# Performance work log

Measured on AMD Instinct MI355X. Metric: run time of the kernel, lower is better.

## Reference

```python
import jax, jax.numpy as jnp
import numpy as np

K = 3          # kernel_size per pseudo-coordinate dim
DIM = 3        # edge_attr dimensionality
M = K ** DIM   # total number of spline kernel weight matrices


def spline_conv(x, src, dst, pseudo, W, Wr, b):
    """Degree-1 open B-spline conv (torch_geometric SplineConv, aggr='mean').
    x: (N, C_in), pseudo: (E, DIM) in [0,1], W: (M, C_in, C_out), Wr: (C_in, C_out), b: (C_out,).
    """
    N, C_in = x.shape
    pos = pseudo * (K - 1)                      # (E, DIM) in [0, K-1]
    i0 = jnp.clip(jnp.floor(pos), 0, K - 2)     # lower knot index per dim
    frac = pos - i0                             # (E, DIM) linear basis fraction
    i0 = i0.astype(jnp.int32)
    strides = jnp.array([1, K, K * K], dtype=jnp.int32)
    xj = x[src]                                 # (E, C_in) irregular gather
    # accumulate basis-weighted neighbor features per (dst node, kernel index)
    acc = jnp.zeros((N * M, C_in), dtype=x.dtype)
    for bits in range(2 ** DIM):                # 8 corners of the linear B-spline support
        off = jnp.array([(bits >> d) & 1 for d in range(DIM)], dtype=jnp.int32)
        w = jnp.prod(jnp.where(off == 1, frac, 1.0 - frac), axis=1)       # (E,)
        kidx = jnp.sum((i0 + off[None, :]) * strides[None, :], axis=1)    # (E,) flat kernel idx
        acc = acc.at[dst * M + kidx].add(w[:, None] * xj)                 # scatter-add
    out = jnp.einsum('nmi,mio->no', acc.reshape(N, M, C_in), W)
    deg = jnp.zeros((N,), x.dtype).at[dst].add(1.0)                        # in-degree
    out = out / jnp.maximum(deg, 1.0)[:, None]                             # mean aggregation
    return out + x @ Wr + b                                                # root weight + bias


def setup_inputs() -> dict:
    key = jax.random.key(0)
    ks = jax.random.split(key, 16)
    N, E = 50000, 800000
    dims = [3, 64, 64, 64]
    inp = {
        "x": jax.random.normal(ks[0], (N, 3), jnp.float32),
        "edge_index": jax.random.randint(ks[1], (2, E), 0, N),
        "edge_attr": jax.random.uniform(ks[2], (E, DIM), dtype=jnp.float32),
    }
    for l in range(3):
        ci, co = dims[l], dims[l + 1]
        inp[f"W{l}"] = jax.random.normal(ks[3 + 3 * l], (M, ci, co), jnp.float32) * (1.0 / np.sqrt(ci * M))
        inp[f"root{l}"] = jax.random.normal(ks[4 + 3 * l], (ci, co), jnp.float32) * (1.0 / np.sqrt(ci))
        inp[f"b{l}"] = jnp.zeros((co,), jnp.float32)
    return inp


def reference(x, edge_index, edge_attr, W0, root0, b0, W1, root1, b1, W2, root2, b2):
    src, dst = edge_index[0], edge_index[1]   # PyG flow: source_to_target
    h = x
    for W, Wr, b in ((W0, root0, b0), (W1, root1, b1), (W2, root2, b2)):
        h = jax.nn.relu(spline_conv(h, src, dst, edge_attr, W, Wr, b))
    return h
```

## Files before the change

### kernel.cpp

```cpp
#include <hip/hip_runtime.h>
#include <cstdint>


typedef __attribute__((ext_vector_type(8))) short short8;
typedef __attribute__((ext_vector_type(4))) float floatx4;

#define AS1 __attribute__((address_space(1)))
#define AS3 __attribute__((address_space(3)))

__device__ inline short f2bf(float f) {
    union { float f; unsigned u; } x; x.f = f;
    unsigned r = x.u + 0x7FFF + ((x.u >> 16) & 1);
    return (short)(r >> 16);
}

__device__ inline float bf2f(unsigned short u) {
    union { unsigned u; float f; } x;
    x.u = ((unsigned)u) << 16;
    return x.f;
}


__global__ void count_kernel(const int* __restrict__ ei, int* __restrict__ count, int E) {
    int e = blockIdx.x * blockDim.x + threadIdx.x;
    if (e < E) atomicAdd(&count[ei[E + e]], 1);
}

__global__ __launch_bounds__(1024) void scan_tile_kernel(const int* __restrict__ count,
                                                         int* __restrict__ row_ptr,
                                                         int* __restrict__ bsum, int N) {
    __shared__ int wsum[16];
    int tid = threadIdx.x, lane = tid & 63, wid = tid >> 6;
    int i = blockIdx.x * 1024 + tid;
    int v = (i < N) ? count[i] : 0;
    int incl = v;
#pragma unroll
    for (int off = 1; off < 64; off <<= 1) {
        int t = __shfl_up(incl, off, 64);
        if (lane >= off) incl += t;
    }
    if (lane == 63) wsum[wid] = incl;
    __syncthreads();
    if (tid < 16) {
        int w = wsum[tid];
#pragma unroll
        for (int off = 1; off < 16; off <<= 1) {
            int t = __shfl_up(w, off, 16);
            if ((tid & 15) >= off) w += t;
        }
        wsum[tid] = w;
    }
    __syncthreads();
    int waveoff = (wid > 0) ? wsum[wid - 1] : 0;
    if (i < N) row_ptr[i] = waveoff + incl - v;
    if (tid == 1023) bsum[blockIdx.x] = waveoff + incl;
}

__global__ __launch_bounds__(64) void scan_bsum_kernel(const int* __restrict__ bsum,
                                                       int* __restrict__ boff,
                                                       int* __restrict__ tot, int nb) {
    int tid = threadIdx.x;
    int v = (tid < nb) ? bsum[tid] : 0;
    int incl = v;
#pragma unroll
    for (int off = 1; off < 64; off <<= 1) {
        int t = __shfl_up(incl, off, 64);
        if (tid >= off) incl += t;
    }
    boff[tid] = incl - v;
    if (tid == 63) tot[0] = incl;
}

__global__ __launch_bounds__(1024) void scan_add_kernel(int* __restrict__ row_ptr,
                                                        const int* __restrict__ boff,
                                                        const int* __restrict__ tot,
                                                        int* __restrict__ cursor, int N) {
    int i = blockIdx.x * 1024 + threadIdx.x;
    if (i < N) {
        int r = row_ptr[i] + boff[blockIdx.x];
        row_ptr[i] = r;
        cursor[i] = r;
    }
    if (i == 0) row_ptr[N] = tot[0];
}

__global__ void basis_sort_kernel(const int* __restrict__ ei, const float* __restrict__ attr,
                                  const int* __restrict__ count, int* __restrict__ cursor,
                                  int* __restrict__ s_meta, float* __restrict__ s_w,
                                  unsigned short* __restrict__ s_wcol, int E) {
    int e = blockIdx.x * blockDim.x + threadIdx.x;
    if (e >= E) return;
    int src = ei[e];
    int dst = ei[E + e];
    float f[3]; int i0[3];
#pragma unroll
    for (int d = 0; d < 3; d++) {
        float pos = attr[e * 3 + d] * 2.0f;
        float fl = floorf(pos);
        fl = fminf(fmaxf(fl, 0.0f), 1.0f);
        i0[d] = (int)fl;
        f[d] = pos - fl;
    }
    int base = i0[0] + 3 * i0[1] + 9 * i0[2];
    float invd = 1.0f / fmaxf((float)count[dst], 1.0f);
    int p = atomicAdd(&cursor[dst], 1);
    s_meta[p] = src | (base << 24);
    float w[8];
#pragma unroll
    for (int c = 0; c < 8; c++) {
        float ww = invd;
#pragma unroll
        for (int d = 0; d < 3; d++) {
            int off = (c >> d) & 1;
            ww *= off ? f[d] : (1.0f - f[d]);
        }
        w[c] = ww;
    }
    floatx4 w03 = {w[0], w[1], w[2], w[3]};
    floatx4 w47 = {w[4], w[5], w[6], w[7]};
    *(floatx4*)(s_w + (size_t)p * 8) = w03;
    *(floatx4*)(s_w + (size_t)p * 8 + 4) = w47;
    unsigned short* wc = s_wcol + (size_t)p * 32;
    short8 z8 = {0, 0, 0, 0, 0, 0, 0, 0};
    *(short8*)(wc) = z8;
    *(short8*)(wc + 8) = z8;
    *(short8*)(wc + 16) = z8;
    *(short8*)(wc + 24) = z8;
#pragma unroll
    for (int c = 0; c < 8; c++) {
        int coff = (c & 1) + 3 * ((c >> 1) & 1) + 9 * (c >> 2);
        wc[base + coff] = (unsigned short)f2bf(w[c]);
    }
}

__global__ void build_wb2(const float* __restrict__ Wa, const float* __restrict__ Ra,
                          unsigned short* __restrict__ wba,
                          const float* __restrict__ Wb, const float* __restrict__ Rb,
                          unsigned short* __restrict__ wbb) {
    int idx0 = blockIdx.x * blockDim.x + threadIdx.x;
    int half = idx0 / (4 * 56 * 64);
    if (half >= 2) return;
    int idx = idx0 - half * (4 * 56 * 64);
    const float* W = half ? Wb : Wa;
    const float* Wr = half ? Rb : Ra;
    unsigned short* wb = half ? wbb : wba;
    int l = idx & 63;
    int c = (idx >> 6) % 56;
    int t = idx / (56 * 64);
    int q = l >> 4, o = t * 16 + (l & 15);
    short8 out;
#pragma unroll
    for (int j = 0; j < 8; j++) {
        int k = c * 32 + q * 8 + j;
        float v = (k < 1728) ? W[(size_t)k * 64 + o] : Wr[(size_t)(k - 1728) * 64 + o];
        out[j] = f2bf(v);
    }
    *(short8*)(wb + (size_t)idx * 8) = out;
}

__global__ __launch_bounds__(256) void layer0_kernel(
    const float* __restrict__ x, const float* __restrict__ W0,
    const float* __restrict__ Wr, const float* __restrict__ bias,
    const int* __restrict__ row_ptr, const int* __restrict__ s_meta,
    const float* __restrict__ s_w, unsigned short* __restrict__ h_out, int N) {
    constexpr int NPB = 32, KT = 84;
    __shared__ __align__(16) float acc[NPB * 2 * KT];
    int tid = threadIdx.x, lane = tid & 63, wv = tid >> 6;
    int n0 = blockIdx.x * NPB;
    for (int k = tid; k < NPB * 2 * KT; k += 256) acc[k] = 0.0f;
    __syncthreads();

    int d = lane >> 5, hl = lane & 31;
    int c = hl / 3, i = hl - c * 3;
    bool act = (hl < 24);
    int cc = act ? c : 0;
    int coff = (c & 1) + 3 * ((c >> 1) & 1) + 9 * (c >> 2);

    for (int g2 = 0; g2 < 8; g2++) {
        int g = wv * 8 + g2;
        int n = n0 + g;
        if (n >= N) continue;
        if (lane < 3) acc[(g * 2) * KT + 81 + lane] = x[(size_t)n * 3 + lane];
        int rs = row_ptr[n], re = row_ptr[n + 1];
        int npairs = (re - rs + 1) >> 1;
        float* accd = &acc[(g * 2 + d) * KT];
        for (int pb = 0; pb < npairs; pb += 4) {
            int metas[4]; float ws_[4], xs_[4];
#pragma unroll
            for (int j = 0; j < 4; j++) {
                int ej = rs + (pb + j) * 2 + d;
                bool v = (pb + j < npairs) && (ej < re);
                int ec = v ? ej : rs;
                metas[j] = s_meta[ec];
                float wv_ = s_w[(size_t)ec * 8 + cc];
                ws_[j] = v ? wv_ : 0.0f;
            }
#pragma unroll
            for (int j = 0; j < 4; j++)
                xs_[j] = x[(size_t)(metas[j] & 0xFFFFFF) * 3 + i];
#pragma unroll
            for (int j = 0; j < 4; j++) {
                int kidx = ((metas[j] >> 24) & 0xF) + coff;
                if (act) accd[kidx * 3 + i] += ws_[j] * xs_[j];
            }
        }
    }
    __syncthreads();

    int o = lane;
    float wreg[KT];
#pragma unroll
    for (int k = 0; k < KT; k++)
        wreg[k] = (k < 81) ? W0[k * 64 + o] : Wr[(k - 81) * 64 + o];
    float bv = bias[o];
    for (int g = wv; g < NPB; g += 4) {
        int n = n0 + g;
        if (n >= N) break;
        float s = bv;
#pragma unroll
        for (int k4 = 0; k4 < KT; k4 += 4) {
            floatx4 a0 = *(const floatx4*)&acc[(g * 2) * KT + k4];
            floatx4 a1 = *(const floatx4*)&acc[(g * 2 + 1) * KT + k4];
            s += (a0.x + a1.x) * wreg[k4] + (a0.y + a1.y) * wreg[k4 + 1]
               + (a0.z + a1.z) * wreg[k4 + 2] + (a0.w + a1.w) * wreg[k4 + 3];
        }
        h_out[(size_t)n * 64 + o] = (unsigned short)f2bf(fmaxf(s, 0.0f));
    }
}

template <bool OUTF32>
__global__ __launch_bounds__(512, 4) void layer64_kernel(
    const unsigned short* __restrict__ h_in, const unsigned short* __restrict__ wb,
    const float* __restrict__ bias, const int* __restrict__ row_ptr,
    const int* __restrict__ s_meta, const unsigned short* __restrict__ s_wcol,
    const unsigned short* __restrict__ zpad, void* __restrict__ h_out, int N) {
    constexpr int NPB = 8;
    constexpr int RGS = 3216;
    __shared__ __align__(16) unsigned short lds[NPB * RGS];
    int tid = threadIdx.x, lane = tid & 63;
    int wvu = __builtin_amdgcn_readfirstlane(tid >> 6);
    int n0 = blockIdx.x * NPB;
    int srow = lane & 15, sgrp = lane >> 4;

    unsigned short* reg = &lds[(size_t)wvu * RGS];
    unsigned short* featL = reg;
    unsigned short* wcolL = reg + 2048;
    int* metaL = (int*)(reg + 3072);

#define STAGE_WCOL(CB) do { \
    _Pragma("unroll") for (int k = 0; k < 2; k++) { \
        int el = (CB) + k * 16 + (lane >> 2); \
        const unsigned short* srcp = (el < dw) \
            ? s_wcol + (size_t)(rs + wbo + el) * 32 + (lane & 3) * 8 \
            : zpad + (lane & 3) * 8; \
        __builtin_amdgcn_global_load_lds((const AS1 unsigned int*)srcp, \
            (AS3 unsigned int*)(wcolL + k * 512), 16, 0, 0); \
    } \
} while (0)

    {
        int n = n0 + wvu;
        if (n >= N) {
            for (int k = lane; k < 1792; k += 64) reg[k] = 0;
        } else {
            {
                short8 z = {0, 0, 0, 0, 0, 0, 0, 0};
#pragma unroll
                for (int s = 0; s < 4; s++)
                    *(short8*)(featL + lane * 8 + s * 512) = z;
            }
            floatx4 facc[2][4];
#pragma unroll
            for (int mt = 0; mt < 2; mt++)
#pragma unroll
                for (int nt = 0; nt < 4; nt++)
                    facc[mt][nt] = (floatx4){0.0f, 0.0f, 0.0f, 0.0f};

            int rs = row_ptr[n], re = row_ptr[n + 1];
            int deg = re - rs;
            for (int wbo = 0; wbo < deg; wbo += 64) {
                int dw = deg - wbo;
                __builtin_amdgcn_global_load_lds(
                    (const AS1 unsigned int*)(s_meta + rs + wbo + lane),
                    (AS3 unsigned int*)metaL, 4, 0, 0);
                STAGE_WCOL(0);
                asm volatile("s_waitcnt vmcnt(0)" ::: "memory");
                int vmax = (dw < 64 ? dw : 64) - 1;
                for (int ch2 = 0; ch2 < 2; ch2++) {
                    int cb = ch2 * 32;
                    if (cb >= dw) break;
                    int nsl = dw - cb; if (nsl > 32) nsl = 32;
                    int ngl = (nsl + 7) >> 3;
                    for (int i = 0; i < ngl; i++) {
                        int el = cb + i * 8 + (lane >> 3);
                        if (el > vmax) el = vmax;
                        int ms = metaL[el] & 0xFFFFFF;
                        int c3 = (lane & 7) ^ (i << 1);
                        const unsigned short* srcp = h_in + (size_t)ms * 64 + c3 * 8;
                        __builtin_amdgcn_global_load_lds(
                            (const AS1 unsigned int*)srcp,
                            (AS3 unsigned int*)(featL + i * 512), 16, 0, 0);
                    }
                    short8 af0, af1;
                    {
                        const unsigned short* wrp = wcolL + (8 * sgrp) * 32 + srow;
#pragma unroll
                        for (int j = 0; j < 8; j++) {
                            af0[j] = (short)wrp[j * 32];
                            af1[j] = (short)wrp[j * 32 + 16];
                        }
                    }
                    if (ch2 == 0 && dw > 32) {
                        asm volatile("s_waitcnt lgkmcnt(0)" ::: "memory");
                        __builtin_amdgcn_sched_barrier(0);
                        STAGE_WCOL(32);
                    }
                    asm volatile("s_waitcnt vmcnt(0)" ::: "memory");
#pragma unroll
                    for (int nt = 0; nt < 4; nt++) {
                        short8 bn;
#pragma unroll
                        for (int jj = 0; jj < 8; jj++) {
                            int e = sgrp * 8 + jj;
                            int g = e * 8 + (((nt * 2) + (srow >> 3)) ^ (sgrp << 1));
                            bn[jj] = (short)featL[g * 8 + (srow & 7)];
                        }
                        facc[0][nt] = __builtin_amdgcn_mfma_f32_16x16x32_bf16(
                            af0, bn, facc[0][nt], 0, 0, 0);
                        facc[1][nt] = __builtin_amdgcn_mfma_f32_16x16x32_bf16(
                            af1, bn, facc[1][nt], 0, 0, 0);
                    }
                }
            }
#pragma unroll
            for (int mt = 0; mt < 2; mt++)
#pragma unroll
                for (int nt = 0; nt < 4; nt++)
#pragma unroll
                    for (int r = 0; r < 4; r++) {
                        int mrow = mt * 16 + sgrp * 4 + r;
                        if (mrow < 27)
                            reg[mrow * 64 + nt * 16 + srow] =
                                (unsigned short)f2bf(facc[mt][nt][r]);
                    }
            reg[1728 + lane] = h_in[(size_t)n * 64 + lane];
        }
    }
#undef STAGE_WCOL
    __syncthreads();

    {
        floatx4 f0 = {0.0f, 0.0f, 0.0f, 0.0f};
        floatx4 f1 = {0.0f, 0.0f, 0.0f, 0.0f};
        if (wvu < 4) {
            int hf = wvu >> 1;
            int tp = wvu & 1;
            const unsigned short* ap = lds + (size_t)(lane & 7) * RGS + ((lane >> 4) * 8);
            const unsigned short* wbp0 = wb + ((size_t)((tp * 2) * 56) * 64 + lane) * 8;
            const unsigned short* wbp1 = wb + ((size_t)((tp * 2 + 1) * 56) * 64 + lane) * 8;
#pragma unroll
            for (int ci = 0; ci < 28; ci++) {
                int c = hf * 28 + ci;
                short8 af = *(const short8*)(ap + c * 32);
                short8 b0 = *(const short8*)(wbp0 + (size_t)c * 64 * 8);
                short8 b1 = *(const short8*)(wbp1 + (size_t)c * 64 * 8);
                f0 = __builtin_amdgcn_mfma_f32_16x16x32_bf16(af, b0, f0, 0, 0, 0);
                f1 = __builtin_amdgcn_mfma_f32_16x16x32_bf16(af, b1, f1, 0, 0, 0);
            }
        }
        __syncthreads();
        if (wvu < 4) {
            float* pfw = (float*)(lds + (size_t)wvu * RGS);
#pragma unroll
            for (int r = 0; r < 4; r++) {
                pfw[r * 64 + lane] = f0[r];
                pfw[256 + r * 64 + lane] = f1[r];
            }
        }
        __syncthreads();
        if (wvu < 4) {
            int t = wvu;
            int o = t * 16 + (lane & 15);
            float bv = bias[o];
            const float* pfA = (const float*)(lds + (size_t)(t >> 1) * RGS)
                             + (t & 1) * 256;
            const float* pfB = (const float*)(lds + (size_t)(2 + (t >> 1)) * RGS)
                             + (t & 1) * 256;
#pragma unroll
            for (int r = 0; r < 4; r++) {
                int m = (lane >> 4) * 4 + r;
                if (m < 8) {
                    int n = n0 + m;
                    if (n < N) {
                        float s = pfA[r * 64 + lane] + pfB[r * 64 + lane];
                        float val = fmaxf(s + bv, 0.0f);
                        if (OUTF32) {
                            ((float*)h_out)[(size_t)n * 64 + o] = val;
                        } else {
                            ((unsigned short*)h_out)[(size_t)n * 64 + o] =
                                (unsigned short)f2bf(val);
                        }
                    }
                }
            }
        }
    }
}

extern "C" void kernel_launch(void* const* d_in, const int* in_sizes, int n_in,
                              void* d_out, int out_size, void* d_ws, size_t ws_size,
                              hipStream_t stream) {
    (void)n_in; (void)out_size; (void)ws_size;
    const float* x    = (const float*)d_in[0];
    const int*   ei   = (const int*)d_in[1];
    const float* attr = (const float*)d_in[2];
    const float* W0 = (const float*)d_in[3];
    const float* R0 = (const float*)d_in[4];
    const float* B0 = (const float*)d_in[5];
    const float* W1 = (const float*)d_in[6];
    const float* R1 = (const float*)d_in[7];
    const float* B1 = (const float*)d_in[8];
    const float* W2 = (const float*)d_in[9];
    const float* R2 = (const float*)d_in[10];
    const float* B2 = (const float*)d_in[11];
    const int N = in_sizes[0] / 3;
    const int E = in_sizes[1] / 2;

    char* ws = (char*)d_ws;
    size_t off = 0;
    auto alloc = [&](size_t bytes) {
        size_t cur = off;
        off = (off + bytes + 255) & ~(size_t)255;
        return cur;
    };
    int* row_ptr = (int*)(ws + alloc((size_t)(N + 1) * 4));
    int* count   = (int*)(ws + alloc((size_t)N * 4));
    int* cursor  = (int*)(ws + alloc((size_t)N * 4));
    int* bsum    = (int*)(ws + alloc(64 * 4));
    int* boff    = (int*)(ws + alloc(64 * 4));
    int* tot     = (int*)(ws + alloc(4));
    unsigned short* zpad = (unsigned short*)(ws + alloc(256));
    int* s_meta  = (int*)(ws + alloc((size_t)E * 4));
    float* s_w   = (float*)(ws + alloc((size_t)E * 8 * 4));
    unsigned short* s_wcol = (unsigned short*)(ws + alloc((size_t)E * 32 * 2));
    unsigned short* h_a  = (unsigned short*)(ws + alloc((size_t)N * 64 * 2));
    unsigned short* h_b  = (unsigned short*)(ws + alloc((size_t)N * 64 * 2));
    unsigned short* wb1  = (unsigned short*)(ws + alloc((size_t)4 * 56 * 64 * 8 * 2));
    unsigned short* wb2  = (unsigned short*)(ws + alloc((size_t)4 * 56 * 64 * 8 * 2));

    int nb = (N + 1023) / 1024;

    hipMemsetAsync(count, 0, (size_t)N * 4, stream);
    hipMemsetAsync(zpad, 0, 256, stream);
    count_kernel<<<(E + 255) / 256, 256, 0, stream>>>(ei, count, E);
    scan_tile_kernel<<<nb, 1024, 0, stream>>>(count, row_ptr, bsum, N);
    scan_bsum_kernel<<<1, 64, 0, stream>>>(bsum, boff, tot, nb);
    scan_add_kernel<<<nb, 1024, 0, stream>>>(row_ptr, boff, tot, cursor, N);
    basis_sort_kernel<<<(E + 255) / 256, 256, 0, stream>>>(ei, attr, count, cursor,
                                                           s_meta, s_w, s_wcol, E);
    build_wb2<<<(2 * 4 * 56 * 64 + 255) / 256, 256, 0, stream>>>(W1, R1, wb1,
                                                                 W2, R2, wb2);

    layer0_kernel<<<(N + 31) / 32, 256, 0, stream>>>(x, W0, R0, B0, row_ptr,
                                                     s_meta, s_w, h_a, N);
    layer64_kernel<false><<<(N + 7) / 8, 512, 0, stream>>>(h_a, wb1, B1, row_ptr,
                                                           s_meta, s_wcol, zpad, h_b, N);
    layer64_kernel<true><<<(N + 7) / 8, 512, 0, stream>>>(h_b, wb2, B2, row_ptr,
                                                          s_meta, s_wcol, zpad, d_out, N);
}
```

Measured before the change: 394.5 us.

## Fuse three-kernel scan into one block and drop fp32 edge weight buffer

Replaces the three-kernel prefix scan (tile scan, block-sum scan, add) with a single-block kernel where each thread serially sums and then writes a contiguous chunk of counts. It also stops writing the fp32 per-edge basis weights (32 bytes per edge) in the sort kernel. Layer 0 instead reads its weight from the bf16 dense s_wcol array using the kernel base index, which cuts write traffic and two launches. In exchange, layer 0 uses bf16-rounded weights, and the single-block scan does strided per-thread reads that coalesce poorly.

```diff
diff --git a/kernel.cpp b/kernel.cpp
--- a/kernel.cpp
+++ b/kernel.cpp
@@ -26,14 +26,19 @@
     if (e < E) atomicAdd(&count[ei[E + e]], 1);
 }
 
-__global__ __launch_bounds__(1024) void scan_tile_kernel(const int* __restrict__ count,
+__global__ __launch_bounds__(1024) void scan_full_kernel(const int* __restrict__ count,
                                                          int* __restrict__ row_ptr,
-                                                         int* __restrict__ bsum, int N) {
+                                                         int* __restrict__ cursor, int N) {
     __shared__ int wsum[16];
     int tid = threadIdx.x, lane = tid & 63, wid = tid >> 6;
-    int i = blockIdx.x * 1024 + tid;
-    int v = (i < N) ? count[i] : 0;
-    int incl = v;
+    int per = (N + 1023) >> 10;
+    int start = tid * per;
+    int sum = 0;
+    for (int k = 0; k < per; k++) {
+        int i = start + k;
+        sum += (i < N) ? count[i] : 0;
+    }
+    int incl = sum;
 #pragma unroll
     for (int off = 1; off < 64; off <<= 1) {
         int t = __shfl_up(incl, off, 64);
@@ -51,42 +56,22 @@
         wsum[tid] = w;
     }
     __syncthreads();
-    int waveoff = (wid > 0) ? wsum[wid - 1] : 0;
-    if (i < N) row_ptr[i] = waveoff + incl - v;
-    if (tid == 1023) bsum[blockIdx.x] = waveoff + incl;
-}
-
-__global__ __launch_bounds__(64) void scan_bsum_kernel(const int* __restrict__ bsum,
-                                                       int* __restrict__ boff,
-                                                       int* __restrict__ tot, int nb) {
-    int tid = threadIdx.x;
-    int v = (tid < nb) ? bsum[tid] : 0;
-    int incl = v;
-#pragma unroll
-    for (int off = 1; off < 64; off <<= 1) {
-        int t = __shfl_up(incl, off, 64);
-        if (tid >= off) incl += t;
-    }
-    boff[tid] = incl - v;
-    if (tid == 63) tot[0] = incl;
-}
-
-__global__ __launch_bounds__(1024) void scan_add_kernel(int* __restrict__ row_ptr,
-                                                        const int* __restrict__ boff,
-                                                        const int* __restrict__ tot,
-                                                        int* __restrict__ cursor, int N) {
-    int i = blockIdx.x * 1024 + threadIdx.x;
-    if (i < N) {
-        int r = row_ptr[i] + boff[blockIdx.x];
-        row_ptr[i] = r;
-        cursor[i] = r;
-    }
-    if (i == 0) row_ptr[N] = tot[0];
+    int base = ((wid > 0) ? wsum[wid - 1] : 0) + incl - sum;
+    int running = base;
+    for (int k = 0; k < per; k++) {
+        int i = start + k;
+        if (i < N) {
+            row_ptr[i] = running;
+            cursor[i] = running;
+            running += count[i];
+        }
+    }
+    if (tid == 1023) row_ptr[N] = base + sum;
 }
 
 __global__ void basis_sort_kernel(const int* __restrict__ ei, const float* __restrict__ attr,
                                   const int* __restrict__ count, int* __restrict__ cursor,
-                                  int* __restrict__ s_meta, float* __restrict__ s_w,
+                                  int* __restrict__ s_meta,
                                   unsigned short* __restrict__ s_wcol, int E) {
     int e = blockIdx.x * blockDim.x + threadIdx.x;
     if (e >= E) return;
@@ -116,10 +101,6 @@
         }
         w[c] = ww;
     }
-    floatx4 w03 = {w[0], w[1], w[2], w[3]};
-    floatx4 w47 = {w[4], w[5], w[6], w[7]};
-    *(floatx4*)(s_w + (size_t)p * 8) = w03;
-    *(floatx4*)(s_w + (size_t)p * 8 + 4) = w47;
     unsigned short* wc = s_wcol + (size_t)p * 32;
     short8 z8 = {0, 0, 0, 0, 0, 0, 0, 0};
     *(short8*)(wc) = z8;
@@ -162,7 +143,7 @@
     const float* __restrict__ x, const float* __restrict__ W0,
     const float* __restrict__ Wr, const float* __restrict__ bias,
     const int* __restrict__ row_ptr, const int* __restrict__ s_meta,
-    const float* __restrict__ s_w, unsigned short* __restrict__ h_out, int N) {
+    const unsigned short* __restrict__ s_wcol, unsigned short* __restrict__ h_out, int N) {
     constexpr int NPB = 32, KT = 84;
     __shared__ __align__(16) float acc[NPB * 2 * KT];
     int tid = threadIdx.x, lane = tid & 63, wv = tid >> 6;
@@ -174,7 +155,7 @@
     int c = hl / 3, i = hl - c * 3;
     bool act = (hl < 24);
     int cc = act ? c : 0;
-    int coff = (c & 1) + 3 * ((c >> 1) & 1) + 9 * (c >> 2);
+    int coff = (cc & 1) + 3 * ((cc >> 1) & 1) + 9 * (cc >> 2);
 
     for (int g2 = 0; g2 < 8; g2++) {
         int g = wv * 8 + g2;
@@ -192,7 +173,8 @@
                 bool v = (pb + j < npairs) && (ej < re);
                 int ec = v ? ej : rs;
                 metas[j] = s_meta[ec];
-                float wv_ = s_w[(size_t)ec * 8 + cc];
+                int base = (metas[j] >> 24) & 0xF;
+                float wv_ = bf2f(s_wcol[(size_t)ec * 32 + base + coff]);
                 ws_[j] = v ? wv_ : 0.0f;
             }
 #pragma unroll
@@ -436,33 +418,25 @@
     int* row_ptr = (int*)(ws + alloc((size_t)(N + 1) * 4));
     int* count   = (int*)(ws + alloc((size_t)N * 4));
     int* cursor  = (int*)(ws + alloc((size_t)N * 4));
-    int* bsum    = (int*)(ws + alloc(64 * 4));
-    int* boff    = (int*)(ws + alloc(64 * 4));
-    int* tot     = (int*)(ws + alloc(4));
     unsigned short* zpad = (unsigned short*)(ws + alloc(256));
     int* s_meta  = (int*)(ws + alloc((size_t)E * 4));
-    float* s_w   = (float*)(ws + alloc((size_t)E * 8 * 4));
     unsigned short* s_wcol = (unsigned short*)(ws + alloc((size_t)E * 32 * 2));
     unsigned short* h_a  = (unsigned short*)(ws + alloc((size_t)N * 64 * 2));
     unsigned short* h_b  = (unsigned short*)(ws + alloc((size_t)N * 64 * 2));
     unsigned short* wb1  = (unsigned short*)(ws + alloc((size_t)4 * 56 * 64 * 8 * 2));
     unsigned short* wb2  = (unsigned short*)(ws + alloc((size_t)4 * 56 * 64 * 8 * 2));
 
-    int nb = (N + 1023) / 1024;
-
     hipMemsetAsync(count, 0, (size_t)N * 4, stream);
     hipMemsetAsync(zpad, 0, 256, stream);
     count_kernel<<<(E + 255) / 256, 256, 0, stream>>>(ei, count, E);
-    scan_tile_kernel<<<nb, 1024, 0, stream>>>(count, row_ptr, bsum, N);
-    scan_bsum_kernel<<<1, 64, 0, stream>>>(bsum, boff, tot, nb);
-    scan_add_kernel<<<nb, 1024, 0, stream>>>(row_ptr, boff, tot, cursor, N);
+    scan_full_kernel<<<1, 1024, 0, stream>>>(count, row_ptr, cursor, N);
     basis_sort_kernel<<<(E + 255) / 256, 256, 0, stream>>>(ei, attr, count, cursor,
-                                                           s_meta, s_w, s_wcol, E);
+                                                           s_meta, s_wcol, E);
     build_wb2<<<(2 * 4 * 56 * 64 + 255) / 256, 256, 0, stream>>>(W1, R1, wb1,
                                                                  W2, R2, wb2);
 
     layer0_kernel<<<(N + 31) / 32, 256, 0, stream>>>(x, W0, R0, B0, row_ptr,
-                                                     s_meta, s_w, h_a, N);
+                                                     s_meta, s_wcol, h_a, N);
     layer64_kernel<false><<<(N + 7) / 8, 512, 0, stream>>>(h_a, wb1, B1, row_ptr,
                                                            s_meta, s_wcol, zpad, h_b, N);
     layer64_kernel<true><<<(N + 7) / 8, 512, 0, stream>>>(h_b, wb2, B2, row_ptr,
```

Result: slower. 508.1 us (+28.8%).
